# Optimization experiments

Measured on AMD Instinct MI355X. Metric: run time of the kernel, lower is better.

The kernel has to match this reference:

```python
import jax, jax.numpy as jnp
import numpy as np

N = 50000   # nodes
F = 32      # num_node_features
EMB = 32    # embedding_size
R = 8       # num_relations
L = 5       # num_layers
E = 400000  # edges


def setup_inputs() -> dict:
    key = jax.random.key(0)
    ks = jax.random.split(key, 12)
    s = 0.1  # weight scale ~ 1/sqrt(fan_in) for stability over 5 residual layers
    return {
        "x": jax.random.normal(ks[0], (N, F), jnp.float32),
        "edge_index": jax.random.randint(ks[1], (2, E), 0, N, jnp.int32),
        "edge_type": jax.random.randint(ks[2], (E,), 0, R, jnp.int32),
        "edge_dist": jax.random.uniform(ks[3], (E,), jnp.float32),
        "fc_W": jax.random.normal(ks[4], (F, EMB), jnp.float32) * s,
        "fc_b": jnp.zeros((EMB,), jnp.float32),
        "rgcn_W": jax.random.normal(ks[5], (L, R, EMB, EMB), jnp.float32) * s,
        "rgcn_root": jax.random.normal(ks[6], (L, EMB, EMB), jnp.float32) * s,
        "rgcn_bias": jnp.zeros((L, EMB), jnp.float32),
        "mlp_W1": jax.random.normal(ks[7], (1 + R, EMB), jnp.float32) * s,
        "mlp_b1": jnp.zeros((EMB,), jnp.float32),
        "mlp_W2": jax.random.normal(ks[8], (EMB, EMB * EMB), jnp.float32) * s,
        "mlp_b2": jnp.zeros((EMB * EMB,), jnp.float32),
        "nn_root": jax.random.normal(ks[9], (L, EMB, EMB), jnp.float32) * s,
        "nn_bias": jnp.zeros((L, EMB), jnp.float32),
    }


def _forward(x, edge_index, edge_type, edge_dist, fc_W, fc_b, rgcn_W, rgcn_root,
             rgcn_bias, mlp_W1, mlp_b1, mlp_W2, mlp_b2, nn_root, nn_bias):
    n = x.shape[0]
    src, dst = edge_index[0], edge_index[1]  # source_to_target flow

    # edge_attr_c = [distance, onehot(edge_type)] : [E, 1+R]
    onehot = jax.nn.one_hot(edge_type, R, dtype=x.dtype)
    eattr = jnp.concatenate([edge_dist[:, None], onehot], axis=1)

    # Shared edge_mlp -> per-edge [EMB, EMB] weight (same for every NNConv layer)
    We = (jax.nn.relu(eattr @ mlp_W1 + mlp_b1) @ mlp_W2 + mlp_b2).reshape(-1, EMB, EMB)

    # degree for NNConv mean aggregation
    deg = jax.ops.segment_sum(jnp.ones_like(edge_dist), dst, num_segments=n)
    denom = jnp.maximum(deg, 1.0)[:, None]

    # per-relation in-degree for RGCN per-relation mean
    rel_cnt = []
    for r in range(R):
        c = jax.ops.segment_sum((edge_type == r).astype(x.dtype), dst, num_segments=n)
        rel_cnt.append(jnp.maximum(c, 1.0)[:, None])

    h = jax.nn.relu(x @ fc_W + fc_b)
    for l in range(L):
        # RGCNConv: root transform + per-relation mean of W_r x_j
        out = h @ rgcn_root[l] + rgcn_bias[l]
        for r in range(R):
            mask_r = (edge_type == r).astype(h.dtype)[:, None]
            msg = (h @ rgcn_W[l, r])[src] * mask_r  # [E, EMB]
            out = out + jax.ops.segment_sum(msg, dst, num_segments=n) / rel_cnt[r]
        h_disc = jax.nn.relu(out)

        # NNConv: x_j @ Theta(e) per edge, mean-aggregated, + root + bias
        msg = jnp.einsum('ei,eio->eo', h[src], We)  # [E, EMB]
        agg = jax.ops.segment_sum(msg, dst, num_segments=n) / denom
        h_cont = jax.nn.relu(h @ nn_root[l] + agg + nn_bias[l])

        h = h + h_disc + h_cont
    return h


def reference(x, edge_index, edge_type, edge_dist, fc_W, fc_b, rgcn_W, rgcn_root,
              rgcn_bias, mlp_W1, mlp_b1, mlp_W2, mlp_b2, nn_root, nn_bias):
    return _forward(x, edge_index, edge_type, edge_dist, fc_W, fc_b, rgcn_W,
                    rgcn_root, rgcn_bias, mlp_W1, mlp_b1, mlp_W2, mlp_b2,
                    nn_root, nn_bias)
```

## Files before the change

kernel.cpp:

```cpp
#include <hip/hip_runtime.h>

#define N_NODES 50000
#define N_EDGES 400000
#define EMB 32
#define NREL 8
#define NLAYER 5
#define NPB 16
#define KROWS 43
#define NCHUNK 196

typedef __attribute__((ext_vector_type(8))) short short8;
typedef __attribute__((ext_vector_type(4))) float f32x4;
typedef __attribute__((ext_vector_type(4))) unsigned int u32x4v;

__device__ __forceinline__ unsigned short f2bf(float f) {
    unsigned u = __float_as_uint(f);
    unsigned r = u + 0x7FFF + ((u >> 16) & 1);
    return (unsigned short)(r >> 16);
}

__device__ __forceinline__ unsigned cvt_pk(float a, float b) {
    unsigned r;
    asm("v_cvt_pk_bf16_f32 %0, %1, %2" : "=v"(r) : "v"(a), "v"(b));
    return r;
}


__global__ __launch_bounds__(256) void zero_kernel(int* __restrict__ p, int n) {
    int i = blockIdx.x * 256 + threadIdx.x;
    if (i < n) p[i] = 0;
}

__global__ __launch_bounds__(256) void hist_kernel(const int* __restrict__ ei,
                                                   const int* __restrict__ et,
                                                   int* __restrict__ deg,
                                                   int* __restrict__ relcnt) {
    int e = blockIdx.x * 256 + threadIdx.x;
    if (e < N_EDGES) {
        int d = ei[N_EDGES + e];
        atomicAdd(&deg[d], 1);
        atomicAdd(&relcnt[d * NREL + et[e]], 1);
    }
}

__global__ __launch_bounds__(256) void bsum_kernel(const int* __restrict__ deg,
                                                   int* __restrict__ bsum) {
    __shared__ int wsum[4];
    int tid = threadIdx.x, lane = tid & 63, w = tid >> 6;
    int i = blockIdx.x * 256 + tid;
    int v = (i < N_NODES) ? deg[i] : 0;
    #pragma unroll
    for (int off = 32; off > 0; off >>= 1) v += __shfl_down(v, off, 64);
    if (lane == 0) wsum[w] = v;
    __syncthreads();
    if (tid == 0) bsum[blockIdx.x] = wsum[0] + wsum[1] + wsum[2] + wsum[3];
}

__global__ __launch_bounds__(256) void boff_kernel(const int* __restrict__ bsum,
                                                   int* __restrict__ boff,
                                                   int* __restrict__ row_ptr) {
    __shared__ int ws[4];
    int tid = threadIdx.x, lane = tid & 63, w = tid >> 6;
    int v = (tid < NCHUNK) ? bsum[tid] : 0;
    int incl = v;
    #pragma unroll
    for (int off = 1; off < 64; off <<= 1) {
        int t = __shfl_up(incl, off, 64);
        if (lane >= off) incl += t;
    }
    if (lane == 63) ws[w] = incl;
    __syncthreads();
    int add = 0;
    for (int j = 0; j < w; j++) add += ws[j];
    if (tid < NCHUNK) boff[tid] = add + incl - v;
    if (tid == 0) row_ptr[N_NODES] = N_EDGES;
}

__global__ __launch_bounds__(256) void rptr_kernel(const int* __restrict__ deg,
                                                   const int* __restrict__ boff,
                                                   int* __restrict__ row_ptr) {
    __shared__ int ws[4];
    int tid = threadIdx.x, lane = tid & 63, w = tid >> 6;
    int i = blockIdx.x * 256 + tid;
    int v = (i < N_NODES) ? deg[i] : 0;
    int incl = v;
    #pragma unroll
    for (int off = 1; off < 64; off <<= 1) {
        int t = __shfl_up(incl, off, 64);
        if (lane >= off) incl += t;
    }
    if (lane == 63) ws[w] = incl;
    __syncthreads();
    int add = boff[blockIdx.x];
    for (int j = 0; j < w; j++) add += ws[j];
    if (i < N_NODES) row_ptr[i] = add + incl - v;
}

__global__ __launch_bounds__(256) void inv_kernel(const int* __restrict__ deg,
                                                  const int* __restrict__ relcnt,
                                                  float* __restrict__ invdeg,
                                                  float* __restrict__ invcnt) {
    int n = blockIdx.x * 256 + threadIdx.x;
    if (n < N_NODES) {
        int d = deg[n];
        invdeg[n] = 1.0f / (float)(d > 0 ? d : 1);
        #pragma unroll
        for (int r = 0; r < NREL; r++) {
            int c = relcnt[n * NREL + r];
            invcnt[n * NREL + r] = 1.0f / (float)(c > 0 ? c : 1);
        }
    }
}

__global__ __launch_bounds__(256) void scatter_kernel(const int* __restrict__ ei,
                                                      const int* __restrict__ et,
                                                      const float* __restrict__ ed,
                                                      const int* __restrict__ row_ptr,
                                                      int* __restrict__ cursor,
                                                      int2* __restrict__ edge2) {
    int e = blockIdx.x * 256 + threadIdx.x;
    if (e < N_EDGES) {
        int d = ei[N_EDGES + e];
        int pos = row_ptr[d] + atomicAdd(&cursor[d], 1);
        edge2[pos] = make_int2(ei[e] | (et[e] << 16), __float_as_int(ed[e]));
    }
}

__global__ __launch_bounds__(256) void wtbf_kernel(const float* __restrict__ W2,
                                                   const float* __restrict__ b2,
                                                   const float* __restrict__ rgcnW,
                                                   const float* __restrict__ rgcnRoot,
                                                   const float* __restrict__ nnRoot,
                                                   unsigned short* __restrict__ WB) {
    int m = blockIdx.x;
    const float* src;
    if (m < 32) src = W2 + (size_t)m * 1024;
    else if (m == 32) src = b2;
    else {
        int t = m - 33, l = t / 10, j = t % 10;
        src = (j < 8) ? rgcnW + (size_t)(l * 8 + j) * 1024
            : (j == 8) ? rgcnRoot + (size_t)l * 1024
                       : nnRoot + (size_t)l * 1024;
    }
    unsigned short* dst = WB + (size_t)m * 1024;
    #pragma unroll
    for (int c = 0; c < 4; c++) {
        int idx = c * 256 + threadIdx.x;
        int o = idx >> 5, k = idx & 31;
        int i = (k >> 1) + ((k & 1) << 4);
        dst[o * 32 + k] = f2bf(src[i * 32 + o]);
    }
}


__global__ __launch_bounds__(256) void fc_kernel(const float* __restrict__ x,
                                                 const float* __restrict__ W,
                                                 const float* __restrict__ b,
                                                 float* __restrict__ h) {
    __shared__ __align__(16) float xt[8][EMB];
    int tid = threadIdx.x;
    int nl = tid >> 5, lane = tid & 31;
    int n0 = blockIdx.x * 8;
    xt[tid >> 5][tid & 31] = x[n0 * EMB + tid];
    __syncthreads();
    float acc = b[lane];
    #pragma unroll
    for (int i = 0; i < EMB; i++) acc += xt[nl][i] * W[i * EMB + lane];
    h[(n0 + nl) * EMB + lane] = fmaxf(acc, 0.0f);
}

__global__ __launch_bounds__(512, 6) void layer_kernel(
    const float* __restrict__ h,
    const int2* __restrict__ edge2,
    const int* __restrict__ row_ptr,
    const float* __restrict__ invdeg,
    const float* __restrict__ invcnt,
    const float* __restrict__ W1,
    const float* __restrict__ b1,
    const unsigned short* __restrict__ WBs,
    const unsigned short* __restrict__ WBl,
    const float* __restrict__ rgcnBias_l,
    const float* __restrict__ nnBias_l,
    float* __restrict__ hout)
{
    __shared__ __align__(16) unsigned short P_lds[NPB][KROWS][EMB];
    __shared__ __align__(16) float wrb2[NREL][32];

    const int tid = threadIdx.x;
    const int n0 = blockIdx.x * NPB;

    if (tid < 256) {
        int r = tid >> 5, i = tid & 31;
        int mm = (i >> 1) + ((i & 1) << 4);
        wrb2[r][i] = W1[(1 + r) * EMB + mm] + b1[mm];
    }
    __syncthreads();

    const int l    = tid & 63;
    const int w    = tid >> 6;
    const int quad = l >> 4;
    const int m    = l & 15;
    const float w10_0 = W1[m];
    const float w10_1 = W1[m + 16];

    for (int pass = 0; pass < 2; ++pass) {
        const int hw = w + pass * 8;
        const int n  = n0 + hw;
        const int pb = row_ptr[n], pe = row_ptr[n + 1];

        f32x4 aP00 = {0.f, 0.f, 0.f, 0.f}, aP01 = {0.f, 0.f, 0.f, 0.f};
        f32x4 aP10 = {0.f, 0.f, 0.f, 0.f}, aP11 = {0.f, 0.f, 0.f, 0.f};
        f32x4 aS0  = {0.f, 0.f, 0.f, 0.f}, aS1  = {0.f, 0.f, 0.f, 0.f};

        for (int c0 = pb; c0 < pe; c0 += 32) {
            const int ebase = c0 + quad * 8;
            const int slack = pe - ebase;
            const int2* ep = edge2 + ebase;
            u32x4v fa0, fa1, fas, fb0, fb1;
            #pragma unroll
            for (int jp = 0; jp < 4; ++jp) {
                int2 ea = ep[2 * jp];
                int2 eb = ep[2 * jp + 1];
                const bool va = (2 * jp)     < slack;
                const bool vb = (2 * jp + 1) < slack;
                int ra = (ea.x >> 16) & 7, rb = (eb.x >> 16) & 7;
                const float2 wa = *(const float2*)&wrb2[ra][2 * m];
                const float2 wb = *(const float2*)&wrb2[rb][2 * m];
                float da = __int_as_float(ea.y), db = __int_as_float(eb.y);
                float hA0 = va ? fmaxf(fmaf(da, w10_0, wa.x), 0.f) : 0.f;
                float hA1 = va ? fmaxf(fmaf(da, w10_1, wa.y), 0.f) : 0.f;
                float hB0 = vb ? fmaxf(fmaf(db, w10_0, wb.x), 0.f) : 0.f;
                float hB1 = vb ? fmaxf(fmaf(db, w10_1, wb.y), 0.f) : 0.f;
                fa0[jp] = cvt_pk(hA0, hB0);
                fa1[jp] = cvt_pk(hA1, hB1);
                float sA = (va && (m == 0 || ra == m - 1)) ? 1.f : 0.f;
                float sB = (vb && (m == 0 || rb == m - 1)) ? 1.f : 0.f;
                fas[jp] = cvt_pk(sA, sB);
                int offa = va ? ((ea.x & 0xFFFF) << 5) + m : m;
                int offb = vb ? ((eb.x & 0xFFFF) << 5) + m : m;
                float bA0 = h[offa], bA1 = h[offa + 16];
                float bB0 = h[offb], bB1 = h[offb + 16];
                fb0[jp] = cvt_pk(bA0, bB0);
                fb1[jp] = cvt_pk(bA1, bB1);
            }
            short8 A0 = __builtin_bit_cast(short8, fa0);
            short8 A1 = __builtin_bit_cast(short8, fa1);
            short8 AS = __builtin_bit_cast(short8, fas);
            short8 B0 = __builtin_bit_cast(short8, fb0);
            short8 B1 = __builtin_bit_cast(short8, fb1);
            aP00 = __builtin_amdgcn_mfma_f32_16x16x32_bf16(A0, B0, aP00, 0, 0, 0);
            aP01 = __builtin_amdgcn_mfma_f32_16x16x32_bf16(A0, B1, aP01, 0, 0, 0);
            aP10 = __builtin_amdgcn_mfma_f32_16x16x32_bf16(A1, B0, aP10, 0, 0, 0);
            aP11 = __builtin_amdgcn_mfma_f32_16x16x32_bf16(A1, B1, aP11, 0, 0, 0);
            aS0  = __builtin_amdgcn_mfma_f32_16x16x32_bf16(AS, B0, aS0, 0, 0, 0);
            aS1  = __builtin_amdgcn_mfma_f32_16x16x32_bf16(AS, B1, aS1, 0, 0, 0);
        }

        const float idg = invdeg[n];
        #pragma unroll
        for (int reg = 0; reg < 4; ++reg) {
            const int row = quad * 4 + reg;
            *(unsigned*)&P_lds[hw][row][2 * m] =
                cvt_pk(aP00[reg] * idg, aP01[reg] * idg);
            *(unsigned*)&P_lds[hw][row + 16][2 * m] =
                cvt_pk(aP10[reg] * idg, aP11[reg] * idg);
            if (row <= 8) {
                const float sc = (row == 0) ? idg : invcnt[n * NREL + row - 1];
                *(unsigned*)&P_lds[hw][32 + row][2 * m] =
                    cvt_pk(aS0[reg] * sc, aS1[reg] * sc);
            }
        }
        if (quad < 2) {
            float h0 = h[n * EMB + m], h1 = h[n * EMB + m + 16];
            *(unsigned*)&P_lds[hw][41 + quad][2 * m] = cvt_pk(h0, h1);
        }
    }
    __syncthreads();

    const int node16 = l & 15;
    const int o0 = l & 15;

    f32x4 accN0 = {0.f, 0.f, 0.f, 0.f}, accN1 = {0.f, 0.f, 0.f, 0.f};
    f32x4 accR0 = {0.f, 0.f, 0.f, 0.f}, accR1 = {0.f, 0.f, 0.f, 0.f};

    #pragma unroll
    for (int j = 0; j < 6; j++) {
        const int rr = w + 8 * j;
        if (rr < KROWS) {
            const unsigned short* Bsrc = (rr < 33) ? (WBs + (size_t)rr * 1024)
                                                   : (WBl + (size_t)(rr - 33) * 1024);
            short8 bf0 = *(const short8*)(Bsrc + o0 * 32 + quad * 8);
            short8 bf1 = *(const short8*)(Bsrc + (o0 + 16) * 32 + quad * 8);
            short8 a = *(const short8*)&P_lds[node16][rr][quad * 8];
            if (rr <= 32 || rr == 42) {
                accN0 = __builtin_amdgcn_mfma_f32_16x16x32_bf16(a, bf0, accN0, 0, 0, 0);
                accN1 = __builtin_amdgcn_mfma_f32_16x16x32_bf16(a, bf1, accN1, 0, 0, 0);
            } else {
                accR0 = __builtin_amdgcn_mfma_f32_16x16x32_bf16(a, bf0, accR0, 0, 0, 0);
                accR1 = __builtin_amdgcn_mfma_f32_16x16x32_bf16(a, bf1, accR1, 0, 0, 0);
            }
        }
    }
    __syncthreads();

    float* RedAll = (float*)&P_lds[0][0][0];
    {
        float* my = RedAll + w * 1024;
        #pragma unroll
        for (int reg = 0; reg < 4; reg++) {
            int nd = quad * 4 + reg;
            my[nd * 32 + o0]            = accN0[reg];
            my[nd * 32 + o0 + 16]       = accN1[reg];
            my[512 + nd * 32 + o0]      = accR0[reg];
            my[512 + nd * 32 + o0 + 16] = accR1[reg];
        }
    }
    __syncthreads();

    {
        const int hw2 = tid >> 5, lane = tid & 31;
        const int n2 = n0 + hw2;
        float sn = 0.0f, sr = 0.0f;
        #pragma unroll
        for (int ww = 0; ww < 8; ww++) {
            sn += RedAll[ww * 1024 + tid];
            sr += RedAll[ww * 1024 + 512 + tid];
        }
        float hd = h[n2 * EMB + lane];
        float o_r = fmaxf(sr + rgcnBias_l[lane], 0.0f);
        float o_n = fmaxf(sn + nnBias_l[lane], 0.0f);
        hout[n2 * EMB + lane] = hd + o_r + o_n;
    }
}


extern "C" void kernel_launch(void* const* d_in, const int* in_sizes, int n_in,
                              void* d_out, int out_size, void* d_ws, size_t ws_size,
                              hipStream_t stream) {
    const float* x        = (const float*)d_in[0];
    const int*   ei       = (const int*)d_in[1];
    const int*   et       = (const int*)d_in[2];
    const float* ed       = (const float*)d_in[3];
    const float* fcW      = (const float*)d_in[4];
    const float* fcb      = (const float*)d_in[5];
    const float* rgcnW    = (const float*)d_in[6];
    const float* rgcnRoot = (const float*)d_in[7];
    const float* rgcnBias = (const float*)d_in[8];
    const float* W1       = (const float*)d_in[9];
    const float* b1       = (const float*)d_in[10];
    const float* W2       = (const float*)d_in[11];
    const float* b2       = (const float*)d_in[12];
    const float* nnRoot   = (const float*)d_in[13];
    const float* nnBias   = (const float*)d_in[14];

    float* ws = (float*)d_ws;
    float* h_a    = ws;  ws += (size_t)N_NODES * EMB;
    float* h_b    = ws;  ws += (size_t)N_NODES * EMB;
    float* invdeg = ws;  ws += (size_t)N_NODES;
    float* invcnt = ws;  ws += (size_t)N_NODES * NREL;
    unsigned short* WB = (unsigned short*)ws;  ws += (size_t)83 * 1024 / 2;
    int2* edge2   = (int2*)ws;     ws += (size_t)N_EDGES * 2;
    int* row_ptr  = (int*)ws;      ws += (size_t)(N_NODES + 1);
    int* bsum     = (int*)ws;      ws += (size_t)NCHUNK;
    int* boff     = (int*)ws;      ws += (size_t)NCHUNK;
    int* deg      = (int*)ws;      ws += (size_t)N_NODES;
    int* relcnt   = (int*)ws;      ws += (size_t)N_NODES * NREL;
    int* cursor   = (int*)ws;      ws += (size_t)N_NODES;
    (void)in_sizes; (void)n_in; (void)out_size; (void)ws_size;

    zero_kernel<<<(10 * N_NODES + 255) / 256, 256, 0, stream>>>(deg, 10 * N_NODES);
    hist_kernel<<<(N_EDGES + 255) / 256, 256, 0, stream>>>(ei, et, deg, relcnt);
    bsum_kernel<<<NCHUNK, 256, 0, stream>>>(deg, bsum);
    inv_kernel<<<(N_NODES + 255) / 256, 256, 0, stream>>>(deg, relcnt, invdeg, invcnt);
    boff_kernel<<<1, 256, 0, stream>>>(bsum, boff, row_ptr);
    rptr_kernel<<<NCHUNK, 256, 0, stream>>>(deg, boff, row_ptr);
    scatter_kernel<<<(N_EDGES + 255) / 256, 256, 0, stream>>>(ei, et, ed, row_ptr,
                                                              cursor, edge2);
    wtbf_kernel<<<83, 256, 0, stream>>>(W2, b2, rgcnW, rgcnRoot, nnRoot, WB);
    fc_kernel<<<N_NODES / 8, 256, 0, stream>>>(x, fcW, fcb, h_a);

    const float* hin = h_a;
    float* houtb = h_b;
    for (int l = 0; l < NLAYER; l++) {
        float* dst = (l == NLAYER - 1) ? (float*)d_out : houtb;
        layer_kernel<<<N_NODES / NPB, 512, 0, stream>>>(
            hin, edge2, row_ptr, invdeg, invcnt, W1, b1,
            WB, WB + (size_t)(33 + l * 10) * 1024,
            rgcnBias + (size_t)l * EMB,
            nnBias + (size_t)l * EMB,
            dst);
        float* old_in = (float*)hin;
        hin = dst;
        houtb = old_in;
    }
}
```

Measured before the change: 453.0 us.

## Pad CSR rows to multiples of eight and balance waves by degree-sorted node pairing

Each node's CSR segment is padded to a multiple of 8 with dummy edges pointing at a zero row, which removes the per-edge validity masks in the gather loop. Within each 16-node block, nodes are sorted by degree and each wave takes one heavy and one light node through a precomputed wave table, so work per wave is more even. Hidden features are stored in an interleaved layout so each lane can load them as float2, and the first edge gathers are issued before the block barrier. In exchange, more edge slots are processed, extra sorting and table-building work runs in preprocessing, and the memory layout becomes more complex.

After: 395.8 us. 12.6% less time.

```diff
diff --git a/kernel.cpp b/kernel.cpp
--- a/kernel.cpp
+++ b/kernel.cpp
@@ -6,8 +6,10 @@
 #define NREL 8
 #define NLAYER 5
 #define NPB 16
+#define NBLK (N_NODES / NPB)
 #define KROWS 43
 #define NCHUNK 196
+#define E2CAP (N_EDGES + 8 * N_NODES)
 
 typedef __attribute__((ext_vector_type(8))) short short8;
 typedef __attribute__((ext_vector_type(4))) float f32x4;
@@ -26,9 +28,14 @@
 }
 
 
-__global__ __launch_bounds__(256) void zero_kernel(int* __restrict__ p, int n) {
+__global__ __launch_bounds__(256) void fill_kernel(int* __restrict__ zeroblk,
+                                                   int2* __restrict__ edge2,
+                                                   float* __restrict__ ha,
+                                                   float* __restrict__ hb) {
     int i = blockIdx.x * 256 + threadIdx.x;
-    if (i < n) p[i] = 0;
+    if (i < E2CAP) edge2[i] = make_int2(N_NODES, 0);
+    if (i < 10 * N_NODES) zeroblk[i] = 0;
+    if (i < EMB) { ha[(size_t)N_NODES * EMB + i] = 0.0f; hb[(size_t)N_NODES * EMB + i] = 0.0f; }
 }
 
 __global__ __launch_bounds__(256) void hist_kernel(const int* __restrict__ ei,
@@ -43,17 +50,47 @@
     }
 }
 
-__global__ __launch_bounds__(256) void bsum_kernel(const int* __restrict__ deg,
-                                                   int* __restrict__ bsum) {
+__device__ __forceinline__ int pdeg_of(int d) {
+    return (d > 0 ? d + 7 : 8) & ~7;
+}
+
+__global__ __launch_bounds__(256) void nodeprep_kernel(const int* __restrict__ deg,
+                                                       const int* __restrict__ relcnt,
+                                                       int* __restrict__ bsum,
+                                                       float* __restrict__ invdeg,
+                                                       float* __restrict__ invcnt,
+                                                       unsigned char* __restrict__ perm) {
     __shared__ int wsum[4];
-    int tid = threadIdx.x, lane = tid & 63, w = tid >> 6;
+    int tid = threadIdx.x, lane = tid & 63, wv = tid >> 6;
     int i = blockIdx.x * 256 + tid;
-    int v = (i < N_NODES) ? deg[i] : 0;
+    int d = (i < N_NODES) ? deg[i] : 0;
+    int v = (i < N_NODES) ? pdeg_of(d) : 0;
     #pragma unroll
     for (int off = 32; off > 0; off >>= 1) v += __shfl_down(v, off, 64);
-    if (lane == 0) wsum[w] = v;
+    if (lane == 0) wsum[wv] = v;
     __syncthreads();
     if (tid == 0) bsum[blockIdx.x] = wsum[0] + wsum[1] + wsum[2] + wsum[3];
+    if (i < N_NODES) {
+        invdeg[i] = 1.0f / (float)(d > 0 ? d : 1);
+        #pragma unroll
+        for (int r = 0; r < NREL; r++) {
+            int c = relcnt[i * NREL + r];
+            invcnt[i * NREL + r] = 1.0f / (float)(c > 0 ? c : 1);
+        }
+    }
+    if (i < NBLK) {
+        int dd[NPB]; unsigned char idx[NPB];
+        #pragma unroll
+        for (int k = 0; k < NPB; k++) { dd[k] = deg[i * NPB + k]; idx[k] = (unsigned char)k; }
+        for (int a = 1; a < NPB; a++) {
+            int dv = dd[a]; unsigned char iv = idx[a];
+            int j = a - 1;
+            while (j >= 0 && dd[j] < dv) { dd[j + 1] = dd[j]; idx[j + 1] = idx[j]; j--; }
+            dd[j + 1] = dv; idx[j + 1] = iv;
+        }
+        #pragma unroll
+        for (int k = 0; k < NPB; k++) perm[i * NPB + k] = idx[k];
+    }
 }
 
 __global__ __launch_bounds__(256) void boff_kernel(const int* __restrict__ bsum,
@@ -73,7 +110,7 @@
     int add = 0;
     for (int j = 0; j < w; j++) add += ws[j];
     if (tid < NCHUNK) boff[tid] = add + incl - v;
-    if (tid == 0) row_ptr[N_NODES] = N_EDGES;
+    if (tid == 0) row_ptr[N_NODES] = ws[0] + ws[1] + ws[2] + ws[3];
 }
 
 __global__ __launch_bounds__(256) void rptr_kernel(const int* __restrict__ deg,
@@ -82,7 +119,7 @@
     __shared__ int ws[4];
     int tid = threadIdx.x, lane = tid & 63, w = tid >> 6;
     int i = blockIdx.x * 256 + tid;
-    int v = (i < N_NODES) ? deg[i] : 0;
+    int v = (i < N_NODES) ? pdeg_of(deg[i]) : 0;
     int incl = v;
     #pragma unroll
     for (int off = 1; off < 64; off <<= 1) {
@@ -94,22 +131,6 @@
     int add = boff[blockIdx.x];
     for (int j = 0; j < w; j++) add += ws[j];
     if (i < N_NODES) row_ptr[i] = add + incl - v;
-}
-
-__global__ __launch_bounds__(256) void inv_kernel(const int* __restrict__ deg,
-                                                  const int* __restrict__ relcnt,
-                                                  float* __restrict__ invdeg,
-                                                  float* __restrict__ invcnt) {
-    int n = blockIdx.x * 256 + threadIdx.x;
-    if (n < N_NODES) {
-        int d = deg[n];
-        invdeg[n] = 1.0f / (float)(d > 0 ? d : 1);
-        #pragma unroll
-        for (int r = 0; r < NREL; r++) {
-            int c = relcnt[n * NREL + r];
-            invcnt[n * NREL + r] = 1.0f / (float)(c > 0 ? c : 1);
-        }
-    }
 }
 
 __global__ __launch_bounds__(256) void scatter_kernel(const int* __restrict__ ei,
@@ -117,12 +138,22 @@
                                                       const float* __restrict__ ed,
                                                       const int* __restrict__ row_ptr,
                                                       int* __restrict__ cursor,
-                                                      int2* __restrict__ edge2) {
+                                                      int2* __restrict__ edge2,
+                                                      const unsigned char* __restrict__ perm,
+                                                      int4* __restrict__ wavetab) {
     int e = blockIdx.x * 256 + threadIdx.x;
     if (e < N_EDGES) {
         int d = ei[N_EDGES + e];
         int pos = row_ptr[d] + atomicAdd(&cursor[d], 1);
         edge2[pos] = make_int2(ei[e] | (et[e] << 16), __float_as_int(ed[e]));
+    }
+    if (e < NBLK * 8) {
+        int b = e >> 3, wv = e & 7;
+        int s0 = perm[b * NPB + wv], s1 = perm[b * NPB + (NPB - 1 - wv)];
+        int nA = b * NPB + s0, nB = b * NPB + s1;
+        int pb0 = row_ptr[nA], pd0 = row_ptr[nA + 1] - pb0;
+        int pb1 = row_ptr[nB], pd1 = row_ptr[nB + 1] - pb1;
+        wavetab[e] = make_int4(s0 | (s1 << 8), pb0, pb1, pd0 | (pd1 << 16));
     }
 }
 
@@ -166,13 +197,150 @@
     float acc = b[lane];
     #pragma unroll
     for (int i = 0; i < EMB; i++) acc += xt[nl][i] * W[i * EMB + lane];
-    h[(n0 + nl) * EMB + lane] = fmaxf(acc, 0.0f);
+    int ol = ((lane & 15) << 1) | (lane >> 4);
+    h[(n0 + nl) * EMB + ol] = fmaxf(acc, 0.0f);
+}
+
+
+__device__ __forceinline__ void gath(const float* __restrict__ h, int4 E, int m,
+                                     float2& ga, float2& gb) {
+    ga = *(const float2*)&h[((E.x & 0xFFFF) << 5) + 2 * m];
+    gb = *(const float2*)&h[((E.z & 0xFFFF) << 5) + 2 * m];
+}
+
+__device__ __forceinline__ void proc_pair(int4 E, float2 ga, float2 gb,
+                                          const float2* wrb2f, float w10_0, float w10_1,
+                                          unsigned selm, int m,
+                                          unsigned& A0s, unsigned& A1s, unsigned& ASs,
+                                          unsigned& B0s, unsigned& B1s) {
+    int ra = (E.x >> 16) & 7, rb = (E.z >> 16) & 7;
+    float2 wa = wrb2f[ra * 16 + m];
+    float2 wb = wrb2f[rb * 16 + m];
+    float da = __int_as_float(E.y), db = __int_as_float(E.w);
+    float hA0 = fmaxf(fmaf(da, w10_0, wa.x), 0.f);
+    float hA1 = fmaxf(fmaf(da, w10_1, wa.y), 0.f);
+    float hB0 = fmaxf(fmaf(db, w10_0, wb.x), 0.f);
+    float hB1 = fmaxf(fmaf(db, w10_1, wb.y), 0.f);
+    A0s = cvt_pk(hA0, hB0);
+    A1s = cvt_pk(hA1, hB1);
+    ASs = cvt_pk((float)((selm >> ra) & 1u), (float)((selm >> rb) & 1u));
+    B0s = cvt_pk(ga.x, gb.x);
+    B1s = cvt_pk(ga.y, gb.y);
+}
+
+__device__ __forceinline__ void mfma6(const unsigned* fa0v, const unsigned* fa1v,
+                                      const unsigned* fasv, const unsigned* fb0v,
+                                      const unsigned* fb1v,
+                                      f32x4& aP00, f32x4& aP01, f32x4& aP10, f32x4& aP11,
+                                      f32x4& aS0, f32x4& aS1) {
+    u32x4v u0 = {fa0v[0], fa0v[1], fa0v[2], fa0v[3]};
+    u32x4v u1 = {fa1v[0], fa1v[1], fa1v[2], fa1v[3]};
+    u32x4v us = {fasv[0], fasv[1], fasv[2], fasv[3]};
+    u32x4v v0 = {fb0v[0], fb0v[1], fb0v[2], fb0v[3]};
+    u32x4v v1 = {fb1v[0], fb1v[1], fb1v[2], fb1v[3]};
+    short8 A0 = __builtin_bit_cast(short8, u0);
+    short8 A1 = __builtin_bit_cast(short8, u1);
+    short8 AS = __builtin_bit_cast(short8, us);
+    short8 B0 = __builtin_bit_cast(short8, v0);
+    short8 B1 = __builtin_bit_cast(short8, v1);
+    aP00 = __builtin_amdgcn_mfma_f32_16x16x32_bf16(A0, B0, aP00, 0, 0, 0);
+    aP01 = __builtin_amdgcn_mfma_f32_16x16x32_bf16(A0, B1, aP01, 0, 0, 0);
+    aP10 = __builtin_amdgcn_mfma_f32_16x16x32_bf16(A1, B0, aP10, 0, 0, 0);
+    aP11 = __builtin_amdgcn_mfma_f32_16x16x32_bf16(A1, B1, aP11, 0, 0, 0);
+    aS0  = __builtin_amdgcn_mfma_f32_16x16x32_bf16(AS, B0, aS0, 0, 0, 0);
+    aS1  = __builtin_amdgcn_mfma_f32_16x16x32_bf16(AS, B1, aS1, 0, 0, 0);
+}
+
+__device__ __forceinline__ void edge_pass(const float* __restrict__ h,
+                                          const int2* __restrict__ edge2,
+                                          const float2* wrb2f,
+                                          int pb, int pe, int quad, int m,
+                                          float w10_0, float w10_1, unsigned selm,
+                                          int4 E0, float2 g0a, float2 g0b,
+                                          f32x4& aP00, f32x4& aP01, f32x4& aP10,
+                                          f32x4& aP11, f32x4& aS0, f32x4& aS1) {
+    {
+        unsigned fa0v[4] = {0,0,0,0}, fa1v[4] = {0,0,0,0}, fasv[4] = {0,0,0,0};
+        unsigned fb0v[4] = {0,0,0,0}, fb1v[4] = {0,0,0,0};
+        proc_pair(E0, g0a, g0b, wrb2f, w10_0, w10_1, selm, m,
+                  fa0v[0], fa1v[0], fasv[0], fb0v[0], fb1v[0]);
+        if (pb + 8 < pe) {
+            int4 E = *(const int4*)&edge2[pb + 8 + quad * 2];
+            float2 ga, gb; gath(h, E, m, ga, gb);
+            proc_pair(E, ga, gb, wrb2f, w10_0, w10_1, selm, m,
+                      fa0v[1], fa1v[1], fasv[1], fb0v[1], fb1v[1]);
+        }
+        if (pb + 16 < pe) {
+            int4 E = *(const int4*)&edge2[pb + 16 + quad * 2];
+            float2 ga, gb; gath(h, E, m, ga, gb);
+            proc_pair(E, ga, gb, wrb2f, w10_0, w10_1, selm, m,
+                      fa0v[2], fa1v[2], fasv[2], fb0v[2], fb1v[2]);
+        }
+        if (pb + 24 < pe) {
+            int4 E = *(const int4*)&edge2[pb + 24 + quad * 2];
+            float2 ga, gb; gath(h, E, m, ga, gb);
+            proc_pair(E, ga, gb, wrb2f, w10_0, w10_1, selm, m,
+                      fa0v[3], fa1v[3], fasv[3], fb0v[3], fb1v[3]);
+        }
+        mfma6(fa0v, fa1v, fasv, fb0v, fb1v, aP00, aP01, aP10, aP11, aS0, aS1);
+    }
+    for (int c0 = pb + 32; c0 < pe; c0 += 32) {
+        unsigned fa0v[4] = {0,0,0,0}, fa1v[4] = {0,0,0,0}, fasv[4] = {0,0,0,0};
+        unsigned fb0v[4] = {0,0,0,0}, fb1v[4] = {0,0,0,0};
+        {
+            int4 E = *(const int4*)&edge2[c0 + quad * 2];
+            float2 ga, gb; gath(h, E, m, ga, gb);
+            proc_pair(E, ga, gb, wrb2f, w10_0, w10_1, selm, m,
+                      fa0v[0], fa1v[0], fasv[0], fb0v[0], fb1v[0]);
+        }
+        if (c0 + 8 < pe) {
+            int4 E = *(const int4*)&edge2[c0 + 8 + quad * 2];
+            float2 ga, gb; gath(h, E, m, ga, gb);
+            proc_pair(E, ga, gb, wrb2f, w10_0, w10_1, selm, m,
+                      fa0v[1], fa1v[1], fasv[1], fb0v[1], fb1v[1]);
+        }
+        if (c0 + 16 < pe) {
+            int4 E = *(const int4*)&edge2[c0 + 16 + quad * 2];
+            float2 ga, gb; gath(h, E, m, ga, gb);
+            proc_pair(E, ga, gb, wrb2f, w10_0, w10_1, selm, m,
+                      fa0v[2], fa1v[2], fasv[2], fb0v[2], fb1v[2]);
+        }
+        if (c0 + 24 < pe) {
+            int4 E = *(const int4*)&edge2[c0 + 24 + quad * 2];
+            float2 ga, gb; gath(h, E, m, ga, gb);
+            proc_pair(E, ga, gb, wrb2f, w10_0, w10_1, selm, m,
+                      fa0v[3], fa1v[3], fasv[3], fb0v[3], fb1v[3]);
+        }
+        mfma6(fa0v, fa1v, fasv, fb0v, fb1v, aP00, aP01, aP10, aP11, aS0, aS1);
+    }
+}
+
+__device__ __forceinline__ void stage_node(unsigned short (*P)[EMB], int quad, int m,
+                                           float idg, const float* __restrict__ invcnt_n,
+                                           const float* __restrict__ hrow,
+                                           const f32x4& aP00, const f32x4& aP01,
+                                           const f32x4& aP10, const f32x4& aP11,
+                                           const f32x4& aS0, const f32x4& aS1) {
+    #pragma unroll
+    for (int reg = 0; reg < 4; ++reg) {
+        const int row = quad * 4 + reg;
+        *(unsigned*)&P[row][2 * m]      = cvt_pk(aP00[reg] * idg, aP01[reg] * idg);
+        *(unsigned*)&P[row + 16][2 * m] = cvt_pk(aP10[reg] * idg, aP11[reg] * idg);
+        if (row <= 8) {
+            const float sc = (row == 0) ? idg : invcnt_n[row - 1];
+            *(unsigned*)&P[32 + row][2 * m] = cvt_pk(aS0[reg] * sc, aS1[reg] * sc);
+        }
+    }
+    if (quad < 2) {
+        float2 hh = *(const float2*)&hrow[2 * m];
+        *(unsigned*)&P[41 + quad][2 * m] = cvt_pk(hh.x, hh.y);
+    }
 }
 
 __global__ __launch_bounds__(512, 6) void layer_kernel(
     const float* __restrict__ h,
     const int2* __restrict__ edge2,
-    const int* __restrict__ row_ptr,
+    const int4* __restrict__ wavetab,
     const float* __restrict__ invdeg,
     const float* __restrict__ invcnt,
     const float* __restrict__ W1,
@@ -181,20 +349,20 @@
     const unsigned short* __restrict__ WBl,
     const float* __restrict__ rgcnBias_l,
     const float* __restrict__ nnBias_l,
-    float* __restrict__ hout)
+    float* __restrict__ hout,
+    int last)
 {
     __shared__ __align__(16) unsigned short P_lds[NPB][KROWS][EMB];
-    __shared__ __align__(16) float wrb2[NREL][32];
+    __shared__ __align__(16) float2 wrb2f[NREL * 16];
 
     const int tid = threadIdx.x;
     const int n0 = blockIdx.x * NPB;
 
-    if (tid < 256) {
-        int r = tid >> 5, i = tid & 31;
-        int mm = (i >> 1) + ((i & 1) << 4);
-        wrb2[r][i] = W1[(1 + r) * EMB + mm] + b1[mm];
-    }
-    __syncthreads();
+    if (tid < 128) {
+        int r = tid >> 4, mi = tid & 15;
+        wrb2f[r * 16 + mi] = make_float2(W1[(1 + r) * EMB + mi] + b1[mi],
+                                         W1[(1 + r) * EMB + mi + 16] + b1[mi + 16]);
+    }
 
     const int l    = tid & 63;
     const int w    = tid >> 6;
@@ -202,86 +370,45 @@
     const int m    = l & 15;
     const float w10_0 = W1[m];
     const float w10_1 = W1[m + 16];
-
-    for (int pass = 0; pass < 2; ++pass) {
-        const int hw = w + pass * 8;
-        const int n  = n0 + hw;
-        const int pb = row_ptr[n], pe = row_ptr[n + 1];
-
-        f32x4 aP00 = {0.f, 0.f, 0.f, 0.f}, aP01 = {0.f, 0.f, 0.f, 0.f};
-        f32x4 aP10 = {0.f, 0.f, 0.f, 0.f}, aP11 = {0.f, 0.f, 0.f, 0.f};
-        f32x4 aS0  = {0.f, 0.f, 0.f, 0.f}, aS1  = {0.f, 0.f, 0.f, 0.f};
-
-        for (int c0 = pb; c0 < pe; c0 += 32) {
-            const int ebase = c0 + quad * 8;
-            const int slack = pe - ebase;
-            const int2* ep = edge2 + ebase;
-            u32x4v fa0, fa1, fas, fb0, fb1;
-            #pragma unroll
-            for (int jp = 0; jp < 4; ++jp) {
-                int2 ea = ep[2 * jp];
-                int2 eb = ep[2 * jp + 1];
-                const bool va = (2 * jp)     < slack;
-                const bool vb = (2 * jp + 1) < slack;
-                int ra = (ea.x >> 16) & 7, rb = (eb.x >> 16) & 7;
-                const float2 wa = *(const float2*)&wrb2[ra][2 * m];
-                const float2 wb = *(const float2*)&wrb2[rb][2 * m];
-                float da = __int_as_float(ea.y), db = __int_as_float(eb.y);
-                float hA0 = va ? fmaxf(fmaf(da, w10_0, wa.x), 0.f) : 0.f;
-                float hA1 = va ? fmaxf(fmaf(da, w10_1, wa.y), 0.f) : 0.f;
-                float hB0 = vb ? fmaxf(fmaf(db, w10_0, wb.x), 0.f) : 0.f;
-                float hB1 = vb ? fmaxf(fmaf(db, w10_1, wb.y), 0.f) : 0.f;
-                fa0[jp] = cvt_pk(hA0, hB0);
-                fa1[jp] = cvt_pk(hA1, hB1);
-                float sA = (va && (m == 0 || ra == m - 1)) ? 1.f : 0.f;
-                float sB = (vb && (m == 0 || rb == m - 1)) ? 1.f : 0.f;
-                fas[jp] = cvt_pk(sA, sB);
-                int offa = va ? ((ea.x & 0xFFFF) << 5) + m : m;
-                int offb = vb ? ((eb.x & 0xFFFF) << 5) + m : m;
-                float bA0 = h[offa], bA1 = h[offa + 16];
-                float bB0 = h[offb], bB1 = h[offb + 16];
-                fb0[jp] = cvt_pk(bA0, bB0);
-                fb1[jp] = cvt_pk(bA1, bB1);
-            }
-            short8 A0 = __builtin_bit_cast(short8, fa0);
-            short8 A1 = __builtin_bit_cast(short8, fa1);
-            short8 AS = __builtin_bit_cast(short8, fas);
-            short8 B0 = __builtin_bit_cast(short8, fb0);
-            short8 B1 = __builtin_bit_cast(short8, fb1);
-            aP00 = __builtin_amdgcn_mfma_f32_16x16x32_bf16(A0, B0, aP00, 0, 0, 0);
-            aP01 = __builtin_amdgcn_mfma_f32_16x16x32_bf16(A0, B1, aP01, 0, 0, 0);
-            aP10 = __builtin_amdgcn_mfma_f32_16x16x32_bf16(A1, B0, aP10, 0, 0, 0);
-            aP11 = __builtin_amdgcn_mfma_f32_16x16x32_bf16(A1, B1, aP11, 0, 0, 0);
-            aS0  = __builtin_amdgcn_mfma_f32_16x16x32_bf16(AS, B0, aS0, 0, 0, 0);
-            aS1  = __builtin_amdgcn_mfma_f32_16x16x32_bf16(AS, B1, aS1, 0, 0, 0);
-        }
-
-        const float idg = invdeg[n];
-        #pragma unroll
-        for (int reg = 0; reg < 4; ++reg) {
-            const int row = quad * 4 + reg;
-            *(unsigned*)&P_lds[hw][row][2 * m] =
-                cvt_pk(aP00[reg] * idg, aP01[reg] * idg);
-            *(unsigned*)&P_lds[hw][row + 16][2 * m] =
-                cvt_pk(aP10[reg] * idg, aP11[reg] * idg);
-            if (row <= 8) {
-                const float sc = (row == 0) ? idg : invcnt[n * NREL + row - 1];
-                *(unsigned*)&P_lds[hw][32 + row][2 * m] =
-                    cvt_pk(aS0[reg] * sc, aS1[reg] * sc);
-            }
-        }
-        if (quad < 2) {
-            float h0 = h[n * EMB + m], h1 = h[n * EMB + m + 16];
-            *(unsigned*)&P_lds[hw][41 + quad][2 * m] = cvt_pk(h0, h1);
-        }
+    const unsigned selm = (m == 0) ? 0xFFu : (m <= 8 ? (1u << (m - 1)) : 0u);
+
+    int4 wt = wavetab[blockIdx.x * 8 + w];
+    const int hw0 = wt.x & 0xFF, hw1 = (wt.x >> 8) & 0xFF;
+    const int pb0 = wt.y, pe0 = wt.y + (wt.w & 0xFFFF);
+    const int pb1 = wt.z, pe1 = wt.z + (int)((unsigned)wt.w >> 16);
+    int4 E0 = *(const int4*)&edge2[pb0 + quad * 2];
+    int4 E1 = *(const int4*)&edge2[pb1 + quad * 2];
+    float2 g0a, g0b, g1a, g1b;
+    gath(h, E0, m, g0a, g0b);
+    gath(h, E1, m, g1a, g1b);
+
+    __syncthreads();
+
+    {
+        f32x4 aP00 = {0,0,0,0}, aP01 = {0,0,0,0}, aP10 = {0,0,0,0}, aP11 = {0,0,0,0};
+        f32x4 aS0 = {0,0,0,0}, aS1 = {0,0,0,0};
+        edge_pass(h, edge2, wrb2f, pb0, pe0, quad, m, w10_0, w10_1, selm,
+                  E0, g0a, g0b, aP00, aP01, aP10, aP11, aS0, aS1);
+        const int n = n0 + hw0;
+        stage_node(P_lds[hw0], quad, m, invdeg[n], invcnt + (size_t)n * NREL,
+                   h + (size_t)n * EMB, aP00, aP01, aP10, aP11, aS0, aS1);
+    }
+    {
+        f32x4 aP00 = {0,0,0,0}, aP01 = {0,0,0,0}, aP10 = {0,0,0,0}, aP11 = {0,0,0,0};
+        f32x4 aS0 = {0,0,0,0}, aS1 = {0,0,0,0};
+        edge_pass(h, edge2, wrb2f, pb1, pe1, quad, m, w10_0, w10_1, selm,
+                  E1, g1a, g1b, aP00, aP01, aP10, aP11, aS0, aS1);
+        const int n = n0 + hw1;
+        stage_node(P_lds[hw1], quad, m, invdeg[n], invcnt + (size_t)n * NREL,
+                   h + (size_t)n * EMB, aP00, aP01, aP10, aP11, aS0, aS1);
     }
     __syncthreads();
 
     const int node16 = l & 15;
     const int o0 = l & 15;
 
-    f32x4 accN0 = {0.f, 0.f, 0.f, 0.f}, accN1 = {0.f, 0.f, 0.f, 0.f};
-    f32x4 accR0 = {0.f, 0.f, 0.f, 0.f}, accR1 = {0.f, 0.f, 0.f, 0.f};
+    f32x4 accN0 = {0,0,0,0}, accN1 = {0,0,0,0};
+    f32x4 accR0 = {0,0,0,0}, accR1 = {0,0,0,0};
 
     #pragma unroll
     for (int j = 0; j < 6; j++) {
@@ -326,10 +453,11 @@
             sn += RedAll[ww * 1024 + tid];
             sr += RedAll[ww * 1024 + 512 + tid];
         }
-        float hd = h[n2 * EMB + lane];
+        const int il = ((lane & 15) << 1) | (lane >> 4);
+        float hd = h[(size_t)n2 * EMB + il];
         float o_r = fmaxf(sr + rgcnBias_l[lane], 0.0f);
         float o_n = fmaxf(sn + nnBias_l[lane], 0.0f);
-        hout[n2 * EMB + lane] = hd + o_r + o_n;
+        hout[(size_t)n2 * EMB + (last ? lane : il)] = hd + o_r + o_n;
     }
 }
 
@@ -354,28 +482,29 @@
     const float* nnBias   = (const float*)d_in[14];
 
     float* ws = (float*)d_ws;
-    float* h_a    = ws;  ws += (size_t)N_NODES * EMB;
-    float* h_b    = ws;  ws += (size_t)N_NODES * EMB;
+    float* h_a    = ws;  ws += (size_t)(N_NODES + 1) * EMB;
+    float* h_b    = ws;  ws += (size_t)(N_NODES + 1) * EMB;
     float* invdeg = ws;  ws += (size_t)N_NODES;
     float* invcnt = ws;  ws += (size_t)N_NODES * NREL;
     unsigned short* WB = (unsigned short*)ws;  ws += (size_t)83 * 1024 / 2;
-    int2* edge2   = (int2*)ws;     ws += (size_t)N_EDGES * 2;
+    int2* edge2   = (int2*)ws;     ws += (size_t)E2CAP * 2;
     int* row_ptr  = (int*)ws;      ws += (size_t)(N_NODES + 1);
     int* bsum     = (int*)ws;      ws += (size_t)NCHUNK;
     int* boff     = (int*)ws;      ws += (size_t)NCHUNK;
     int* deg      = (int*)ws;      ws += (size_t)N_NODES;
     int* relcnt   = (int*)ws;      ws += (size_t)N_NODES * NREL;
     int* cursor   = (int*)ws;      ws += (size_t)N_NODES;
+    unsigned char* perm = (unsigned char*)ws;  ws += (size_t)NBLK * NPB / 4;
+    int4* wavetab = (int4*)ws;     ws += (size_t)NBLK * 8 * 4;
     (void)in_sizes; (void)n_in; (void)out_size; (void)ws_size;
 
-    zero_kernel<<<(10 * N_NODES + 255) / 256, 256, 0, stream>>>(deg, 10 * N_NODES);
+    fill_kernel<<<(E2CAP + 255) / 256, 256, 0, stream>>>(deg, edge2, h_a, h_b);
     hist_kernel<<<(N_EDGES + 255) / 256, 256, 0, stream>>>(ei, et, deg, relcnt);
-    bsum_kernel<<<NCHUNK, 256, 0, stream>>>(deg, bsum);
-    inv_kernel<<<(N_NODES + 255) / 256, 256, 0, stream>>>(deg, relcnt, invdeg, invcnt);
+    nodeprep_kernel<<<NCHUNK, 256, 0, stream>>>(deg, relcnt, bsum, invdeg, invcnt, perm);
     boff_kernel<<<1, 256, 0, stream>>>(bsum, boff, row_ptr);
     rptr_kernel<<<NCHUNK, 256, 0, stream>>>(deg, boff, row_ptr);
     scatter_kernel<<<(N_EDGES + 255) / 256, 256, 0, stream>>>(ei, et, ed, row_ptr,
-                                                              cursor, edge2);
+                                                              cursor, edge2, perm, wavetab);
     wtbf_kernel<<<83, 256, 0, stream>>>(W2, b2, rgcnW, rgcnRoot, nnRoot, WB);
     fc_kernel<<<N_NODES / 8, 256, 0, stream>>>(x, fcW, fcb, h_a);
 
@@ -383,12 +512,12 @@
     float* houtb = h_b;
     for (int l = 0; l < NLAYER; l++) {
         float* dst = (l == NLAYER - 1) ? (float*)d_out : houtb;
-        layer_kernel<<<N_NODES / NPB, 512, 0, stream>>>(
-            hin, edge2, row_ptr, invdeg, invcnt, W1, b1,
+        layer_kernel<<<NBLK, 512, 0, stream>>>(
+            hin, edge2, wavetab, invdeg, invcnt, W1, b1,
             WB, WB + (size_t)(33 + l * 10) * 1024,
             rgcnBias + (size_t)l * EMB,
             nnBias + (size_t)l * EMB,
-            dst);
+            dst, (l == NLAYER - 1) ? 1 : 0);
         float* old_in = (float*)hin;
         hin = dst;
         houtb = old_in;
```
